# Kernel optimization log

Hardware: AMD Instinct MI355X
Metric: run time of the kernel (lower is better)

Reference implementation:

```python
import jax, jax.numpy as jnp
import numpy as np

TEMP = 0.1   # args.temperature
EPS = 1e-8   # torch CosineSimilarity eps
T, B, E, N = 512, 64, 1024, 128  # tlen, bz, embsize, nnegs


def setup_inputs() -> dict:
    key = jax.random.key(0)
    k1, k2, k3, k4, k5 = jax.random.split(key, 5)
    return {
        "index": jax.random.randint(k1, (T,), 0, B),
        "z1": jax.random.normal(k2, (T, B, E), dtype=jnp.float32),
        "z2": jax.random.normal(k3, (T, B, E), dtype=jnp.float32),
        "neg_sentence": jax.random.randint(k4, (T, N), 0, T),
        "neg_word": jax.random.randint(k5, (T, N), 0, B),
    }


def _cos_last(a, b):
    # cosine similarity along the last axis with torch-style eps clamping
    num = jnp.sum(a * b, axis=-1)
    na = jnp.maximum(jnp.sqrt(jnp.sum(a * a, axis=-1)), EPS)
    nb = jnp.maximum(jnp.sqrt(jnp.sum(b * b, axis=-1)), EPS)
    return num / (na * nb)


def reference(index, z1, z2, neg_sentence, neg_word):
    # z1, z2: [T, B, E]; index: [T]; neg_*: [T, N]
    t_idx = jnp.arange(z1.shape[0])
    orig = z1[t_idx, index]            # [T, E]  anchor per step
    adv = z2[t_idx, index]             # [T, E]  positive per step
    negs = z1[neg_sentence, neg_word]  # [T, N, E] random negatives

    # positive: CosineSimilarity(dim=1) on [1,E] tensors -> cosine over E
    pos = jnp.exp(_cos_last(orig, adv) / TEMP)  # [T]

    # negative: faithful to torch cossim(negs[1,N,E], orig[1,E]) with dim=1:
    # orig broadcasts to [1,N,E]; cosine is taken over the N axis, per feature e.
    n = negs.shape[1]
    dot = orig * jnp.sum(negs, axis=1)                        # [T, E]
    norm_negs = jnp.sqrt(jnp.sum(negs * negs, axis=1))        # [T, E]
    norm_orig = jnp.sqrt(jnp.asarray(n, orig.dtype)) * jnp.abs(orig)  # [T, E]
    cos_neg = dot / (jnp.maximum(norm_negs, EPS) * jnp.maximum(norm_orig, EPS))
    den = jnp.sum(jnp.exp(cos_neg / TEMP), axis=1)            # [T]

    # sum over the batch loop of -log(num/den)
    loss = jnp.sum(-jnp.log(pos / den))
    return loss
```

## Files before the change

### kernel.cpp

```cpp
#include <hip/hip_runtime.h>
#include <math.h>

#define TT 512
#define BB 64
#define EE 1024
#define NN 128
#define TEMP 0.1f
#define EPSF 1e-8f

__global__ __launch_bounds__(1024) void contloss_main(
    const int*   __restrict__ index,
    const float* __restrict__ z1,
    const float* __restrict__ z2,
    const int*   __restrict__ neg_s,
    const int*   __restrict__ neg_w,
    float*       __restrict__ per_t)
{
    const int t = blockIdx.x;
    const int e = threadIdx.x;

    __shared__ int rowoff[NN];
    __shared__ float4 red[16];

    if (e < NN) {
        int s = neg_s[t * NN + e];
        int w = neg_w[t * NN + e];
        rowoff[e] = (s * BB + w) * EE;
    }
    __syncthreads();

    const int idx = index[t];
    const size_t anchor = ((size_t)t * BB + (size_t)idx) * EE;
    const float orig = z1[anchor + e];
    const float adv  = z2[anchor + e];

    float s1 = 0.f, s2 = 0.f;
#pragma unroll 4
    for (int j = 0; j < NN; ++j) {
        float v = z1[rowoff[j] + e];
        s1 += v;
        s2 += v * v;
    }

    const float dotv  = orig * s1;
    const float nnorm = sqrtf(s2);
    const float onorm = sqrtf((float)NN) * fabsf(orig);
    const float cosn  = dotv / (fmaxf(nnorm, EPSF) * fmaxf(onorm, EPSF));
    float v0 = expf(cosn * (1.0f / TEMP));
    float v1 = orig * adv;
    float v2 = orig * orig;
    float v3 = adv * adv;

    for (int off = 32; off > 0; off >>= 1) {
        v0 += __shfl_xor(v0, off, 64);
        v1 += __shfl_xor(v1, off, 64);
        v2 += __shfl_xor(v2, off, 64);
        v3 += __shfl_xor(v3, off, 64);
    }
    const int lane = e & 63;
    const int wid  = e >> 6;
    if (lane == 0) red[wid] = make_float4(v0, v1, v2, v3);
    __syncthreads();

    if (e < 16) {
        float4 r = red[e];
        float a0 = r.x, a1 = r.y, a2 = r.z, a3 = r.w;
        for (int off = 8; off > 0; off >>= 1) {
            a0 += __shfl_xor(a0, off, 64);
            a1 += __shfl_xor(a1, off, 64);
            a2 += __shfl_xor(a2, off, 64);
            a3 += __shfl_xor(a3, off, 64);
        }
        if (e == 0) {
            const float den  = a0;
            const float na   = fmaxf(sqrtf(a2), EPSF);
            const float nb   = fmaxf(sqrtf(a3), EPSF);
            const float cosp = a1 / (na * nb);
            per_t[t] = -cosp * (1.0f / TEMP) + logf(den);
        }
    }
}

__global__ __launch_bounds__(512) void contloss_reduce(
    const float* __restrict__ per_t, float* __restrict__ out)
{
    const int tid = threadIdx.x;
    float v = per_t[tid];
    for (int off = 32; off > 0; off >>= 1) v += __shfl_xor(v, off, 64);

    __shared__ float red[8];
    const int lane = tid & 63, wid = tid >> 6;
    if (lane == 0) red[wid] = v;
    __syncthreads();
    if (tid < 8) {
        float a = red[tid];
        for (int off = 4; off > 0; off >>= 1) a += __shfl_xor(a, off, 64);
        if (tid == 0) out[0] = a;
    }
}

extern "C" void kernel_launch(void* const* d_in, const int* in_sizes, int n_in,
                              void* d_out, int out_size, void* d_ws, size_t ws_size,
                              hipStream_t stream) {
    const int*   index = (const int*)  d_in[0];
    const float* z1    = (const float*)d_in[1];
    const float* z2    = (const float*)d_in[2];
    const int*   neg_s = (const int*)  d_in[3];
    const int*   neg_w = (const int*)  d_in[4];
    float* out   = (float*)d_out;
    float* per_t = (float*)d_ws;

    contloss_main<<<TT, 1024, 0, stream>>>(index, z1, z2, neg_s, neg_w, per_t);
    contloss_reduce<<<1, 512, 0, stream>>>(per_t, out);
}
```

Baseline: 260.9 us.

## Vectorize negative-row gathers with float4 and split rows across four thread groups

Each thread now loads float4 chunks of the gathered negative rows. The 1024 threads are split into four groups of 256, and each group accumulates a quarter of the 128 negatives. Partial sums are combined through shared memory, and the first 256 threads finish the per-feature cosine and positive terms. This is meant to cut the number of load instructions and raise the number of independent memory requests in flight, at the cost of 32KB of shared memory and an extra barrier.

```diff
diff --git a/kernel.cpp b/kernel.cpp
--- a/kernel.cpp
+++ b/kernel.cpp
@@ -16,40 +16,68 @@
     const int*   __restrict__ neg_w,
     float*       __restrict__ per_t)
 {
-    const int t = blockIdx.x;
-    const int e = threadIdx.x;
+    const int t   = blockIdx.x;
+    const int tid = threadIdx.x;
+    const int sub = tid & 255;
+    const int grp = tid >> 8;
 
-    __shared__ int rowoff[NN];
+    __shared__ int    rowoff[NN];
+    __shared__ float4 part1[4][256];
+    __shared__ float4 part2[4][256];
     __shared__ float4 red[16];
 
-    if (e < NN) {
-        int s = neg_s[t * NN + e];
-        int w = neg_w[t * NN + e];
-        rowoff[e] = (s * BB + w) * EE;
+    if (tid < NN) {
+        const int s = neg_s[t * NN + tid];
+        const int w = neg_w[t * NN + tid];
+        rowoff[tid] = (s * BB + w) * EE;
     }
     __syncthreads();
 
-    const int idx = index[t];
-    const size_t anchor = ((size_t)t * BB + (size_t)idx) * EE;
-    const float orig = z1[anchor + e];
-    const float adv  = z2[anchor + e];
+    float4 s1 = make_float4(0.f, 0.f, 0.f, 0.f);
+    float4 s2 = make_float4(0.f, 0.f, 0.f, 0.f);
+#pragma unroll 8
+    for (int j = grp; j < NN; j += 4) {
+        const float4 v = *reinterpret_cast<const float4*>(z1 + rowoff[j] + 4 * sub);
+        s1.x += v.x; s1.y += v.y; s1.z += v.z; s1.w += v.w;
+        s2.x += v.x * v.x; s2.y += v.y * v.y; s2.z += v.z * v.z; s2.w += v.w * v.w;
+    }
+    part1[grp][sub] = s1;
+    part2[grp][sub] = s2;
+    __syncthreads();
 
-    float s1 = 0.f, s2 = 0.f;
-#pragma unroll 4
-    for (int j = 0; j < NN; ++j) {
-        float v = z1[rowoff[j] + e];
-        s1 += v;
-        s2 += v * v;
+    float v0 = 0.f, v1 = 0.f, v2 = 0.f, v3 = 0.f;
+    if (tid < 256) {
+        float4 a1 = part1[0][tid];
+        float4 a2 = part2[0][tid];
+#pragma unroll
+        for (int g = 1; g < 4; ++g) {
+            const float4 p1 = part1[g][tid];
+            const float4 p2 = part2[g][tid];
+            a1.x += p1.x; a1.y += p1.y; a1.z += p1.z; a1.w += p1.w;
+            a2.x += p2.x; a2.y += p2.y; a2.z += p2.z; a2.w += p2.w;
+        }
+        const int idx = index[t];
+        const size_t anchor = ((size_t)t * BB + (size_t)idx) * EE;
+        const float4 og = *reinterpret_cast<const float4*>(z1 + anchor + 4 * tid);
+        const float4 ad = *reinterpret_cast<const float4*>(z2 + anchor + 4 * tid);
+
+        const float sqn = sqrtf((float)NN);
+        const float og_[4] = {og.x, og.y, og.z, og.w};
+        const float ad_[4] = {ad.x, ad.y, ad.z, ad.w};
+        const float a1_[4] = {a1.x, a1.y, a1.z, a1.w};
+        const float a2_[4] = {a2.x, a2.y, a2.z, a2.w};
+#pragma unroll
+        for (int c = 0; c < 4; ++c) {
+            const float nnorm = sqrtf(a2_[c]);
+            const float onorm = sqn * fabsf(og_[c]);
+            const float cosn  = (og_[c] * a1_[c]) /
+                                (fmaxf(nnorm, EPSF) * fmaxf(onorm, EPSF));
+            v0 += expf(cosn * (1.0f / TEMP));
+            v1 += og_[c] * ad_[c];
+            v2 += og_[c] * og_[c];
+            v3 += ad_[c] * ad_[c];
+        }
     }
-
-    const float dotv  = orig * s1;
-    const float nnorm = sqrtf(s2);
-    const float onorm = sqrtf((float)NN) * fabsf(orig);
-    const float cosn  = dotv / (fmaxf(nnorm, EPSF) * fmaxf(onorm, EPSF));
-    float v0 = expf(cosn * (1.0f / TEMP));
-    float v1 = orig * adv;
-    float v2 = orig * orig;
-    float v3 = adv * adv;
 
     for (int off = 32; off > 0; off >>= 1) {
         v0 += __shfl_xor(v0, off, 64);
@@ -57,13 +85,13 @@
         v2 += __shfl_xor(v2, off, 64);
         v3 += __shfl_xor(v3, off, 64);
     }
-    const int lane = e & 63;
-    const int wid  = e >> 6;
+    const int lane = tid & 63;
+    const int wid  = tid >> 6;
     if (lane == 0) red[wid] = make_float4(v0, v1, v2, v3);
     __syncthreads();
 
-    if (e < 16) {
-        float4 r = red[e];
+    if (tid < 16) {
+        float4 r = red[tid];
         float a0 = r.x, a1 = r.y, a2 = r.z, a3 = r.w;
         for (int off = 8; off > 0; off >>= 1) {
             a0 += __shfl_xor(a0, off, 64);
@@ -71,7 +99,7 @@
             a2 += __shfl_xor(a2, off, 64);
             a3 += __shfl_xor(a3, off, 64);
         }
-        if (e == 0) {
+        if (tid == 0) {
             const float den  = a0;
             const float na   = fmaxf(sqrtf(a2), EPSF);
             const float nb   = fmaxf(sqrtf(a3), EPSF);
```

Result: no change. 259.0 us (-0.7%).
